# Performance work log

Measured on AMD Instinct MI355X. Metric: run time of the kernel, lower is better.

## Reference

```python
import jax, jax.numpy as jnp
import numpy as np

B, S, D, H = 1, 2048, 2048, 32
HD = D // H  # head_dim = 64
FF = 4 * D
EPS = 1e-5


def _alibi_slopes(n_heads):
    # standard ALiBi slopes for power-of-2 head counts: 2^(-8i/n)
    return np.array([2.0 ** (-8.0 * (i + 1) / n_heads) for i in range(n_heads)], np.float32)


def setup_inputs() -> dict:
    key = jax.random.key(0)
    ks = jax.random.split(key, 16)
    s = 0.02
    x = jax.random.normal(ks[0], (B, S, D), jnp.float32)
    # alibi bias [B, H, 1, S], broadcast over query positions (HF views alibi as (b, h, 1, kv_len))
    slopes = _alibi_slopes(H)
    alibi_np = slopes[:, None, None] * np.arange(S, dtype=np.float32)[None, None, :]
    alibi = jnp.broadcast_to(jnp.asarray(alibi_np), (B, H, 1, S))
    # additive causal mask [1, 1, S, S]
    causal = np.tril(np.ones((S, S), bool))
    attention_mask = jnp.asarray(np.where(causal, 0.0, -1e9).astype(np.float32))[None, None]
    p = lambda k, shp: s * jax.random.normal(k, shp, jnp.float32)
    return {
        "x": x,
        "alibi": alibi,
        "attention_mask": attention_mask,
        "ln1_g": jnp.ones((D,), jnp.float32), "ln1_b": jnp.zeros((D,), jnp.float32),
        "ln2_g": jnp.ones((D,), jnp.float32), "ln2_b": jnp.zeros((D,), jnp.float32),
        "wqkv": p(ks[1], (D, 3 * D)), "bqkv": jnp.zeros((3 * D,), jnp.float32),
        "wo": p(ks[2], (D, D)), "bo": jnp.zeros((D,), jnp.float32),
        "w1": p(ks[3], (D, FF)), "b1": jnp.zeros((FF,), jnp.float32),
        "w2": p(ks[4], (FF, D)), "b2": jnp.zeros((D,), jnp.float32),
    }


def _layernorm(h, g, b):
    m = h.mean(-1, keepdims=True)
    v = ((h - m) ** 2).mean(-1, keepdims=True)
    return (h - m) * jax.lax.rsqrt(v + EPS) * g + b


def reference(x, alibi, attention_mask, ln1_g, ln1_b, ln2_g, ln2_b,
              wqkv, bqkv, wo, bo, w1, b1, w2, b2):
    b, s, d = x.shape
    inv_norm = 1.0 / np.sqrt(HD).astype(np.float32)
    # --- input layernorm ---
    h = _layernorm(x, ln1_g, ln1_b)
    # --- fused QKV ---
    qkv = h @ wqkv + bqkv
    q, k, v = jnp.split(qkv, 3, axis=-1)
    q = q.reshape(b, s, H, HD).transpose(0, 2, 1, 3)  # [b, h, s, hd]
    k = k.reshape(b, s, H, HD).transpose(0, 2, 1, 3)
    v = v.reshape(b, s, H, HD).transpose(0, 2, 1, 3)
    # --- ALiBi-biased attention (HF falcon alibi path) ---
    scores = jnp.einsum("bhqd,bhkd->bhqk", q, k)          # [b, h, s, s]
    logits = (scores + alibi) * inv_norm + attention_mask  # alibi broadcasts over q dim
    probs = jax.nn.softmax(logits, axis=-1)
    ctx = jnp.einsum("bhqk,bhkd->bhqd", probs, v)
    ctx = ctx.transpose(0, 2, 1, 3).reshape(b, s, d)
    attn_out = ctx @ wo + bo
    # --- residual, post-attn layernorm, MLP (non-parallel falcon-rw layout) ---
    res = x + attn_out
    h2 = _layernorm(res, ln2_g, ln2_b)
    mlp = jax.nn.gelu(h2 @ w1 + b1, approximate=False) @ w2 + b2
    return res + mlp
```

## Files before the change

kernel.cpp:

```cpp
#include <hip/hip_runtime.h>
#include <hip/hip_bf16.h>
#include <cstdint>
#include <cstddef>

static constexpr int Sq  = 2048;
static constexpr int Dm  = 2048;
static constexpr int NH  = 32;
static constexpr int HDm = 64;
static constexpr int FFm = 8192;

typedef __bf16 bf16x8 __attribute__((ext_vector_type(8)));
typedef float  f32x4  __attribute__((ext_vector_type(4)));

__device__ __forceinline__ void async_ld16(const void* g, void* l) {
  __builtin_amdgcn_global_load_lds((const __attribute__((address_space(1))) void*)g,
                                   (__attribute__((address_space(3))) void*)l, 16, 0, 0);
}

__global__ __launch_bounds__(256)
void tcast_kernel(const float* __restrict__ in, __hip_bfloat16* __restrict__ out,
                  int K, int N) {
  __shared__ float tile[64][65];
  const int tc = blockIdx.x * 64;
  const int tr = blockIdx.y * 64;
  const int cx = threadIdx.x & 63;
  const int ry = threadIdx.x >> 6;
#pragma unroll
  for (int i = 0; i < 16; ++i) {
    int r = ry + i * 4;
    tile[r][cx] = in[(size_t)(tr + r) * N + tc + cx];
  }
  __syncthreads();
#pragma unroll
  for (int i = 0; i < 16; ++i) {
    int r = ry + i * 4;
    out[(size_t)(tc + r) * K + tr + cx] = __float2bfloat16(tile[cx][r]);
  }
}

__global__ __launch_bounds__(256)
void ln_kernel(const float* __restrict__ x, const float* __restrict__ g,
               const float* __restrict__ b, __hip_bfloat16* __restrict__ out) {
  __shared__ float red[4];
  const int t = threadIdx.x;
  const float* xr = x + (size_t)blockIdx.x * Dm;
  float v[8];
  float s = 0.f;
#pragma unroll
  for (int i = 0; i < 8; ++i) { v[i] = xr[t + i * 256]; s += v[i]; }
#pragma unroll
  for (int off = 32; off > 0; off >>= 1) s += __shfl_down(s, off, 64);
  if ((t & 63) == 0) red[t >> 6] = s;
  __syncthreads();
  const float mean = (red[0] + red[1] + red[2] + red[3]) * (1.f / Dm);
  __syncthreads();
  float vs = 0.f;
#pragma unroll
  for (int i = 0; i < 8; ++i) { float d = v[i] - mean; vs += d * d; }
#pragma unroll
  for (int off = 32; off > 0; off >>= 1) vs += __shfl_down(vs, off, 64);
  if ((t & 63) == 0) red[t >> 6] = vs;
  __syncthreads();
  const float inv = rsqrtf((red[0] + red[1] + red[2] + red[3]) * (1.f / Dm) + 1e-5f);
  __hip_bfloat16* orow = out + (size_t)blockIdx.x * Dm;
#pragma unroll
  for (int i = 0; i < 8; ++i) {
    int c = t + i * 256;
    orow[c] = __float2bfloat16((v[i] - mean) * inv * g[c] + b[c]);
  }
}

template <int EPI>
__global__ __launch_bounds__(256)
void gemm_kernel(const __hip_bfloat16* __restrict__ A,
                 const __hip_bfloat16* __restrict__ Bt,
                 int N, int K,
                 const float* __restrict__ bias,
                 const float* __restrict__ addsrc,
                 float* __restrict__ outf,
                 __hip_bfloat16* __restrict__ outb,
                 __hip_bfloat16* __restrict__ qo,
                 __hip_bfloat16* __restrict__ ko,
                 __hip_bfloat16* __restrict__ vo) {
  __shared__ __align__(16) __hip_bfloat16 As[128 * 32];
  __shared__ __align__(16) __hip_bfloat16 Bs[128 * 32];
  const int t = threadIdx.x;
  const int lane = t & 63, w = t >> 6, quad = lane >> 4, l16 = lane & 15;
  const int bn = blockIdx.x, bm = blockIdx.y;
  const int wm = (w & 1) * 64, wn = (w >> 1) * 64;
  const __hip_bfloat16* Abase = A + (size_t)bm * 128 * K;
  const __hip_bfloat16* Bbase = Bt + (size_t)bn * 128 * K;
  f32x4 acc[4][4] = {};
  for (int k0 = 0; k0 < K; k0 += 32) {
#pragma unroll
    for (int j = 0; j < 2; ++j) {
      int c = j * 256 + t;
      int row = c >> 2;
      int swz = (c & 3) ^ (row & 3);
      async_ld16(Abase + (size_t)row * K + k0 + swz * 8, As + c * 8);
      async_ld16(Bbase + (size_t)row * K + k0 + swz * 8, Bs + c * 8);
    }
    __syncthreads();
    bf16x8 af[4], bfv[4];
#pragma unroll
    for (int i = 0; i < 4; ++i) {
      int row = wm + i * 16 + l16;
      af[i] = *(const bf16x8*)(As + row * 32 + (quad ^ (row & 3)) * 8);
    }
#pragma unroll
    for (int i = 0; i < 4; ++i) {
      int row = wn + i * 16 + l16;
      bfv[i] = *(const bf16x8*)(Bs + row * 32 + (quad ^ (row & 3)) * 8);
    }
#pragma unroll
    for (int mt = 0; mt < 4; ++mt)
#pragma unroll
      for (int nt = 0; nt < 4; ++nt)
        acc[mt][nt] = __builtin_amdgcn_mfma_f32_16x16x32_bf16(af[mt], bfv[nt], acc[mt][nt], 0, 0, 0);
    __syncthreads();
  }
#pragma unroll
  for (int mt = 0; mt < 4; ++mt) {
#pragma unroll
    for (int nt = 0; nt < 4; ++nt) {
      const int n = bn * 128 + wn + nt * 16 + l16;
      const float bz = bias[n];
#pragma unroll
      for (int r = 0; r < 4; ++r) {
        const int m = bm * 128 + wm + mt * 16 + quad * 4 + r;
        float val = acc[mt][nt][r] + bz;
        if constexpr (EPI == 0) {
          int which = n >> 11, d2 = n & 2047;
          int hh = d2 >> 6, hd = d2 & 63;
          if (which == 0)
            qo[((size_t)hh * Sq + m) * HDm + hd] = __float2bfloat16(val * 0.125f);
          else if (which == 1)
            ko[((size_t)hh * Sq + m) * HDm + hd] = __float2bfloat16(val);
          else
            vo[((size_t)hh * HDm + hd) * Sq + m] = __float2bfloat16(val);
        } else if constexpr (EPI == 1) {
          outf[(size_t)m * N + n] = addsrc[(size_t)m * N + n] + val;
        } else {
          float gg = 0.5f * val * (1.0f + erff(val * 0.70710678118654752f));
          outb[(size_t)m * N + n] = __float2bfloat16(gg);
        }
      }
    }
  }
}

__global__ __launch_bounds__(256)
void attn_kernel(const __hip_bfloat16* __restrict__ qb,
                 const __hip_bfloat16* __restrict__ kb,
                 const __hip_bfloat16* __restrict__ vt,
                 const float* __restrict__ alibi,
                 __hip_bfloat16* __restrict__ ctx) {
  __shared__ __align__(16) __hip_bfloat16 Kl[64 * 64];
  __shared__ __align__(16) __hip_bfloat16 Vl[64 * 64];
  __shared__ __align__(16) __hip_bfloat16 Pl[4][16 * 64];
  const int qblk = blockIdx.x, h = blockIdx.y;
  const int t = threadIdx.x, w = t >> 6, lane = t & 63, quad = lane >> 4, l16 = lane & 15;
  const __hip_bfloat16* qh = qb + (size_t)h * Sq * HDm;
  const __hip_bfloat16* kh = kb + (size_t)h * Sq * HDm;
  const __hip_bfloat16* vh = vt + (size_t)h * HDm * Sq;
  const float* al = alibi + (size_t)h * Sq;
  const int qr0 = qblk * 64 + w * 16;
  const bf16x8 qa0 = *(const bf16x8*)(qh + (size_t)(qr0 + l16) * HDm + quad * 8);
  const bf16x8 qa1 = *(const bf16x8*)(qh + (size_t)(qr0 + l16) * HDm + 32 + quad * 8);
  f32x4 o[4] = {};
  float m_i[4], l_i[4];
#pragma unroll
  for (int r = 0; r < 4; ++r) { m_i[r] = -3e38f; l_i[r] = 0.f; }
  for (int kbk = 0; kbk <= qblk; ++kbk) {
    __syncthreads();
#pragma unroll
    for (int j = 0; j < 2; ++j) {
      int c = j * 256 + t;
      int row = c >> 3;
      int swz = (c & 7) ^ (row & 7);
      async_ld16(kh + (size_t)(kbk * 64 + row) * HDm + swz * 8, Kl + c * 8);
      async_ld16(vh + (size_t)row * Sq + kbk * 64 + swz * 8, Vl + c * 8);
    }
    __syncthreads();
    f32x4 sf[4];
    const f32x4 zero = {};
#pragma unroll
    for (int nt = 0; nt < 4; ++nt) {
      int row = nt * 16 + l16;
      bf16x8 kf0 = *(const bf16x8*)(Kl + row * 64 + ((quad ^ (row & 7)) << 3));
      bf16x8 kf1 = *(const bf16x8*)(Kl + row * 64 + (((4 + quad) ^ (row & 7)) << 3));
      sf[nt] = __builtin_amdgcn_mfma_f32_16x16x32_bf16(qa0, kf0, zero, 0, 0, 0);
      sf[nt] = __builtin_amdgcn_mfma_f32_16x16x32_bf16(qa1, kf1, sf[nt], 0, 0, 0);
    }
    const bool diag = (kbk == qblk);
    float mrow[4] = {-3e38f, -3e38f, -3e38f, -3e38f};
#pragma unroll
    for (int nt = 0; nt < 4; ++nt) {
      const float ab = al[kbk * 64 + nt * 16 + l16] * 0.125f;
      const int kcol = nt * 16 + l16;
#pragma unroll
      for (int r = 0; r < 4; ++r) {
        float vv = sf[nt][r] + ab;
        if (diag && kcol > w * 16 + quad * 4 + r) vv = -3e38f;
        sf[nt][r] = vv;
        mrow[r] = fmaxf(mrow[r], vv);
      }
    }
#pragma unroll
    for (int off = 8; off > 0; off >>= 1)
#pragma unroll
      for (int r = 0; r < 4; ++r)
        mrow[r] = fmaxf(mrow[r], __shfl_xor(mrow[r], off, 64));
    float alpha[4], rs[4], p[4][4];
#pragma unroll
    for (int r = 0; r < 4; ++r) {
      float mn = fmaxf(m_i[r], mrow[r]);
      alpha[r] = __expf(m_i[r] - mn);
      m_i[r] = mn;
    }
#pragma unroll
    for (int nt = 0; nt < 4; ++nt)
#pragma unroll
      for (int r = 0; r < 4; ++r) p[nt][r] = __expf(sf[nt][r] - m_i[r]);
#pragma unroll
    for (int r = 0; r < 4; ++r) rs[r] = p[0][r] + p[1][r] + p[2][r] + p[3][r];
#pragma unroll
    for (int off = 8; off > 0; off >>= 1)
#pragma unroll
      for (int r = 0; r < 4; ++r) rs[r] += __shfl_xor(rs[r], off, 64);
#pragma unroll
    for (int r = 0; r < 4; ++r) l_i[r] = l_i[r] * alpha[r] + rs[r];
#pragma unroll
    for (int dt = 0; dt < 4; ++dt)
#pragma unroll
      for (int r = 0; r < 4; ++r) o[dt][r] *= alpha[r];
    __hip_bfloat16* pw = &Pl[w][0];
#pragma unroll
    for (int nt = 0; nt < 4; ++nt)
#pragma unroll
      for (int r = 0; r < 4; ++r) {
        int prow = quad * 4 + r;
        int e = nt * 16 + l16;
        int c16 = e >> 3;
        pw[prow * 64 + ((c16 ^ (prow & 7)) << 3) + (e & 7)] = __float2bfloat16(p[nt][r]);
      }
    asm volatile("s_waitcnt lgkmcnt(0)" ::: "memory");
    const bf16x8 pa0 = *(const bf16x8*)(pw + l16 * 64 + ((quad ^ (l16 & 7)) << 3));
    const bf16x8 pa1 = *(const bf16x8*)(pw + l16 * 64 + (((4 + quad) ^ (l16 & 7)) << 3));
#pragma unroll
    for (int dt = 0; dt < 4; ++dt) {
      int row = dt * 16 + l16;
      bf16x8 v0 = *(const bf16x8*)(Vl + row * 64 + ((quad ^ (row & 7)) << 3));
      bf16x8 v1 = *(const bf16x8*)(Vl + row * 64 + (((4 + quad) ^ (row & 7)) << 3));
      o[dt] = __builtin_amdgcn_mfma_f32_16x16x32_bf16(pa0, v0, o[dt], 0, 0, 0);
      o[dt] = __builtin_amdgcn_mfma_f32_16x16x32_bf16(pa1, v1, o[dt], 0, 0, 0);
    }
  }
#pragma unroll
  for (int dt = 0; dt < 4; ++dt)
#pragma unroll
    for (int r = 0; r < 4; ++r) {
      int srow = qblk * 64 + w * 16 + quad * 4 + r;
      ctx[(size_t)srow * Dm + h * HDm + dt * 16 + l16] =
          __float2bfloat16(o[dt][r] / l_i[r]);
    }
}

extern "C" void kernel_launch(void* const* d_in, const int* in_sizes, int n_in,
                              void* d_out, int out_size, void* d_ws, size_t ws_size,
                              hipStream_t stream) {
  const float* x     = (const float*)d_in[0];
  const float* alibi = (const float*)d_in[1];
  const float* ln1g  = (const float*)d_in[3];
  const float* ln1b  = (const float*)d_in[4];
  const float* ln2g  = (const float*)d_in[5];
  const float* ln2b  = (const float*)d_in[6];
  const float* wqkv  = (const float*)d_in[7];
  const float* bqkv  = (const float*)d_in[8];
  const float* wo    = (const float*)d_in[9];
  const float* bo    = (const float*)d_in[10];
  const float* w1    = (const float*)d_in[11];
  const float* b1    = (const float*)d_in[12];
  const float* w2    = (const float*)d_in[13];
  const float* b2    = (const float*)d_in[14];
  float* out = (float*)d_out;

  char* p = (char*)d_ws;
  auto alloc = [&](size_t bytes) {
    char* r = p;
    p += (bytes + 255) & ~(size_t)255;
    return r;
  };
  constexpr size_t SD2 = (size_t)Sq * Dm * 2;
  char* R2 = alloc((size_t)FFm * Dm * 2);
  char* R1 = alloc(4 * SD2);
  __hip_bfloat16* hb   = (__hip_bfloat16*)alloc(SD2);
  float*          resb = (float*)alloc((size_t)Sq * Dm * 4);

  __hip_bfloat16* wqkvT = (__hip_bfloat16*)R2;
  __hip_bfloat16* w1T   = (__hip_bfloat16*)R2;
  __hip_bfloat16* w2T   = (__hip_bfloat16*)R2;
  __hip_bfloat16* qbuf  = (__hip_bfloat16*)(R1 + 0 * SD2);
  __hip_bfloat16* kbuf  = (__hip_bfloat16*)(R1 + 1 * SD2);
  __hip_bfloat16* vtbuf = (__hip_bfloat16*)(R1 + 2 * SD2);
  __hip_bfloat16* ctxb  = (__hip_bfloat16*)(R1 + 3 * SD2);
  __hip_bfloat16* woT   = (__hip_bfloat16*)(R1 + 0 * SD2);
  __hip_bfloat16* t1b   = (__hip_bfloat16*)R1;

  tcast_kernel<<<dim3(3 * Dm / 64, Dm / 64), 256, 0, stream>>>(wqkv, wqkvT, Dm, 3 * Dm);
  ln_kernel<<<Sq, 256, 0, stream>>>(x, ln1g, ln1b, hb);
  gemm_kernel<0><<<dim3(3 * Dm / 128, Sq / 128), 256, 0, stream>>>(
      hb, wqkvT, 3 * Dm, Dm, bqkv, nullptr, nullptr, nullptr, qbuf, kbuf, vtbuf);
  tcast_kernel<<<dim3(FFm / 64, Dm / 64), 256, 0, stream>>>(w1, w1T, Dm, FFm);
  attn_kernel<<<dim3(Sq / 64, NH), 256, 0, stream>>>(qbuf, kbuf, vtbuf, alibi, ctxb);
  tcast_kernel<<<dim3(Dm / 64, Dm / 64), 256, 0, stream>>>(wo, woT, Dm, Dm);
  gemm_kernel<1><<<dim3(Dm / 128, Sq / 128), 256, 0, stream>>>(
      ctxb, woT, Dm, Dm, bo, x, resb, nullptr, nullptr, nullptr, nullptr);
  ln_kernel<<<Sq, 256, 0, stream>>>(resb, ln2g, ln2b, hb);
  gemm_kernel<2><<<dim3(FFm / 128, Sq / 128), 256, 0, stream>>>(
      hb, w1T, FFm, Dm, b1, nullptr, nullptr, t1b, nullptr, nullptr, nullptr);
  tcast_kernel<<<dim3(Dm / 64, FFm / 64), 256, 0, stream>>>(w2, w2T, FFm, Dm);
  gemm_kernel<1><<<dim3(Dm / 128, Sq / 128), 256, 0, stream>>>(
      t1b, w2T, Dm, FFm, b2, resb, out, nullptr, nullptr, nullptr, nullptr);
}
```

Baseline: 793.1 us.

## Double-buffer GEMM LDS staging, change swizzle, and split-K the final MLP GEMM

The GEMM kernel now double-buffers its A/B shared-memory tiles so the next K-slice's async loads overlap the current slice's MFMAs, and it drops one barrier per iteration. The LDS swizzle changes from XOR to a rotation pattern. The final FFN down-projection (K=8192, only 256 blocks) is split-K in two: one half writes fp32 with the residual and bias, the other writes a bf16 partial that a new add kernel folds in. This raises parallelism for that GEMM at the cost of an extra pass over the output and bf16 rounding of half the partial sum.

```diff
diff --git a/kernel.cpp b/kernel.cpp
--- a/kernel.cpp
+++ b/kernel.cpp
@@ -74,62 +74,74 @@
 __global__ __launch_bounds__(256)
 void gemm_kernel(const __hip_bfloat16* __restrict__ A,
                  const __hip_bfloat16* __restrict__ Bt,
-                 int N, int K,
+                 int N, int K, int Ksub,
                  const float* __restrict__ bias,
                  const float* __restrict__ addsrc,
                  float* __restrict__ outf,
                  __hip_bfloat16* __restrict__ outb,
                  __hip_bfloat16* __restrict__ qo,
                  __hip_bfloat16* __restrict__ ko,
-                 __hip_bfloat16* __restrict__ vo) {
-  __shared__ __align__(16) __hip_bfloat16 As[128 * 32];
-  __shared__ __align__(16) __hip_bfloat16 Bs[128 * 32];
+                 __hip_bfloat16* __restrict__ vo,
+                 __hip_bfloat16* __restrict__ po) {
+  __shared__ __align__(16) __hip_bfloat16 As[2][128 * 32];
+  __shared__ __align__(16) __hip_bfloat16 Bs[2][128 * 32];
   const int t = threadIdx.x;
   const int lane = t & 63, w = t >> 6, quad = lane >> 4, l16 = lane & 15;
-  const int bn = blockIdx.x, bm = blockIdx.y;
+  const int bn = blockIdx.x, bm = blockIdx.y, bz = blockIdx.z;
   const int wm = (w & 1) * 64, wn = (w >> 1) * 64;
   const __hip_bfloat16* Abase = A + (size_t)bm * 128 * K;
   const __hip_bfloat16* Bbase = Bt + (size_t)bn * 128 * K;
-  f32x4 acc[4][4] = {};
-  for (int k0 = 0; k0 < K; k0 += 32) {
+  const int kBeg = bz * Ksub, kEnd = kBeg + Ksub;
+
+  auto stage = [&](int b, int k0) {
 #pragma unroll
     for (int j = 0; j < 2; ++j) {
       int c = j * 256 + t;
       int row = c >> 2;
-      int swz = (c & 3) ^ (row & 3);
-      async_ld16(Abase + (size_t)row * K + k0 + swz * 8, As + c * 8);
-      async_ld16(Bbase + (size_t)row * K + k0 + swz * 8, Bs + c * 8);
-    }
+      int p = c & 3;
+      int g = (p - (row >> 1)) & 3;
+      async_ld16(Abase + (size_t)row * K + k0 + g * 8, &As[b][c * 8]);
+      async_ld16(Bbase + (size_t)row * K + k0 + g * 8, &Bs[b][c * 8]);
+    }
+  };
+
+  f32x4 acc[4][4] = {};
+  stage(0, kBeg);
+  int buf = 0;
+  for (int k0 = kBeg; k0 < kEnd; k0 += 32, buf ^= 1) {
     __syncthreads();
+    if (k0 + 32 < kEnd) stage(buf ^ 1, k0 + 32);
     bf16x8 af[4], bfv[4];
 #pragma unroll
     for (int i = 0; i < 4; ++i) {
       int row = wm + i * 16 + l16;
-      af[i] = *(const bf16x8*)(As + row * 32 + (quad ^ (row & 3)) * 8);
+      int p = (quad + (row >> 1)) & 3;
+      af[i] = *(const bf16x8*)(&As[buf][row * 32 + p * 8]);
     }
 #pragma unroll
     for (int i = 0; i < 4; ++i) {
       int row = wn + i * 16 + l16;
-      bfv[i] = *(const bf16x8*)(Bs + row * 32 + (quad ^ (row & 3)) * 8);
+      int p = (quad + (row >> 1)) & 3;
+      bfv[i] = *(const bf16x8*)(&Bs[buf][row * 32 + p * 8]);
     }
 #pragma unroll
     for (int mt = 0; mt < 4; ++mt)
 #pragma unroll
       for (int nt = 0; nt < 4; ++nt)
         acc[mt][nt] = __builtin_amdgcn_mfma_f32_16x16x32_bf16(af[mt], bfv[nt], acc[mt][nt], 0, 0, 0);
-    __syncthreads();
   }
 #pragma unroll
   for (int mt = 0; mt < 4; ++mt) {
 #pragma unroll
     for (int nt = 0; nt < 4; ++nt) {
       const int n = bn * 128 + wn + nt * 16 + l16;
-      const float bz = bias[n];
+      const float bz2 = bias[n];
 #pragma unroll
       for (int r = 0; r < 4; ++r) {
         const int m = bm * 128 + wm + mt * 16 + quad * 4 + r;
-        float val = acc[mt][nt][r] + bz;
+        float val = acc[mt][nt][r];
         if constexpr (EPI == 0) {
+          val += bz2;
           int which = n >> 11, d2 = n & 2047;
           int hh = d2 >> 6, hd = d2 & 63;
           if (which == 0)
@@ -139,14 +151,29 @@
           else
             vo[((size_t)hh * HDm + hd) * Sq + m] = __float2bfloat16(val);
         } else if constexpr (EPI == 1) {
-          outf[(size_t)m * N + n] = addsrc[(size_t)m * N + n] + val;
-        } else {
+          outf[(size_t)m * N + n] = addsrc[(size_t)m * N + n] + bz2 + val;
+        } else if constexpr (EPI == 2) {
+          val += bz2;
           float gg = 0.5f * val * (1.0f + erff(val * 0.70710678118654752f));
           outb[(size_t)m * N + n] = __float2bfloat16(gg);
+        } else {
+          if (bz == 0)
+            outf[(size_t)m * N + n] = addsrc[(size_t)m * N + n] + bz2 + val;
+          else
+            po[(size_t)m * N + n] = __float2bfloat16(val);
         }
       }
     }
   }
+}
+
+__global__ __launch_bounds__(256)
+void addp_kernel(float* __restrict__ out, const __hip_bfloat16* __restrict__ p) {
+  const int i = (blockIdx.x * 256 + threadIdx.x) * 4;
+  float4 o = *(const float4*)(out + i);
+  const __hip_bfloat16* pp = p + i;
+  o.x += (float)pp[0]; o.y += (float)pp[1]; o.z += (float)pp[2]; o.w += (float)pp[3];
+  *(float4*)(out + i) = o;
 }
 
 __global__ __launch_bounds__(256)
@@ -306,20 +333,22 @@
   __hip_bfloat16* ctxb  = (__hip_bfloat16*)(R1 + 3 * SD2);
   __hip_bfloat16* woT   = (__hip_bfloat16*)(R1 + 0 * SD2);
   __hip_bfloat16* t1b   = (__hip_bfloat16*)R1;
+  __hip_bfloat16* part  = hb;
 
   tcast_kernel<<<dim3(3 * Dm / 64, Dm / 64), 256, 0, stream>>>(wqkv, wqkvT, Dm, 3 * Dm);
   ln_kernel<<<Sq, 256, 0, stream>>>(x, ln1g, ln1b, hb);
   gemm_kernel<0><<<dim3(3 * Dm / 128, Sq / 128), 256, 0, stream>>>(
-      hb, wqkvT, 3 * Dm, Dm, bqkv, nullptr, nullptr, nullptr, qbuf, kbuf, vtbuf);
+      hb, wqkvT, 3 * Dm, Dm, Dm, bqkv, nullptr, nullptr, nullptr, qbuf, kbuf, vtbuf, nullptr);
   tcast_kernel<<<dim3(FFm / 64, Dm / 64), 256, 0, stream>>>(w1, w1T, Dm, FFm);
   attn_kernel<<<dim3(Sq / 64, NH), 256, 0, stream>>>(qbuf, kbuf, vtbuf, alibi, ctxb);
   tcast_kernel<<<dim3(Dm / 64, Dm / 64), 256, 0, stream>>>(wo, woT, Dm, Dm);
   gemm_kernel<1><<<dim3(Dm / 128, Sq / 128), 256, 0, stream>>>(
-      ctxb, woT, Dm, Dm, bo, x, resb, nullptr, nullptr, nullptr, nullptr);
+      ctxb, woT, Dm, Dm, Dm, bo, x, resb, nullptr, nullptr, nullptr, nullptr, nullptr);
   ln_kernel<<<Sq, 256, 0, stream>>>(resb, ln2g, ln2b, hb);
   gemm_kernel<2><<<dim3(FFm / 128, Sq / 128), 256, 0, stream>>>(
-      hb, w1T, FFm, Dm, b1, nullptr, nullptr, t1b, nullptr, nullptr, nullptr);
+      hb, w1T, FFm, Dm, Dm, b1, nullptr, nullptr, t1b, nullptr, nullptr, nullptr, nullptr);
   tcast_kernel<<<dim3(Dm / 64, FFm / 64), 256, 0, stream>>>(w2, w2T, FFm, Dm);
-  gemm_kernel<1><<<dim3(Dm / 128, Sq / 128), 256, 0, stream>>>(
-      t1b, w2T, Dm, FFm, b2, resb, out, nullptr, nullptr, nullptr, nullptr);
-}
+  gemm_kernel<3><<<dim3(Dm / 128, Sq / 128, 2), 256, 0, stream>>>(
+      t1b, w2T, Dm, FFm, FFm / 2, b2, resb, out, nullptr, nullptr, nullptr, nullptr, part);
+  addp_kernel<<<(Sq * Dm) / 1024, 256, 0, stream>>>(out, part);
+}
```

Result: faster. 715.5 us (-9.8%).
